# Kernel optimization log

Hardware: AMD Instinct MI355X
Metric: run time of the kernel (lower is better)

Reference implementation:

```python
import jax, jax.numpy as jnp
import numpy as np

B, S, D = 4, 2048, 1024
H = 16
DH = D // H  # 64


def setup_inputs() -> dict:
    key = jax.random.key(0)
    ks = jax.random.split(key, 9)
    s = 0.02
    return {
        "x": jax.random.normal(ks[0], (B, S, D), dtype=jnp.float32),
        "Wq": jax.random.normal(ks[1], (D, D), dtype=jnp.float32) * s,
        "bq": jnp.zeros((D,), dtype=jnp.float32),
        "Wk": jax.random.normal(ks[2], (D, D), dtype=jnp.float32) * s,
        "bk": jnp.zeros((D,), dtype=jnp.float32),
        "Wv": jax.random.normal(ks[3], (D, D), dtype=jnp.float32) * s,
        "bv": jnp.zeros((D,), dtype=jnp.float32),
        "Wp": jax.random.normal(ks[4], (D, D), dtype=jnp.float32) * s,
        "bp": jnp.zeros((D,), dtype=jnp.float32),
    }


def reference(x, Wq, bq, Wk, bk, Wv, bv, Wp, bp):
    b, s, d = x.shape
    # projections (torch Linear: x @ W.T + b)
    q = (x @ Wq.T + bq).reshape(b, s, H, DH).transpose(0, 2, 1, 3)   # [B,H,S,DH]
    # quirk faithful to source: key viewed as (B,S,DH,H) then transpose(1,3) -> [B,H,DH,S]
    k = (x @ Wk.T + bk).reshape(b, s, DH, H).transpose(0, 3, 2, 1)   # [B,H,DH,S]
    v = (x @ Wv.T + bv).reshape(b, s, H, DH).transpose(0, 2, 1, 3)   # [B,H,S,DH]

    scale = 1.0 / np.sqrt(DH).astype(np.float32)
    scores = jnp.einsum('bhqd,bhds->bhqs', q, k) * scale             # [B,H,S,S]
    causal = jnp.tril(jnp.ones((s, s), dtype=bool))
    scores = jnp.where(causal, scores, -jnp.inf)
    attn = jax.nn.softmax(scores, axis=-1)
    out = jnp.einsum('bhqs,bhsd->bhqd', attn, v)                      # [B,H,S,DH]
    out = out.transpose(0, 2, 1, 3).reshape(b, s, d)                  # [B,S,D]
    return out @ Wp.T + bp
```

## Files before the change

kernel.cpp:

```cpp
#include <hip/hip_runtime.h>
#include <cstdint>

#define B_  4
#define S_  2048
#define D_  1024
#define H_  16
#define DH_ 64

typedef unsigned short u16;
typedef __attribute__((ext_vector_type(8))) __bf16 bf16x8;
typedef __attribute__((ext_vector_type(4))) float f32x4;
typedef __attribute__((ext_vector_type(2))) uint32_t u32x2;

__device__ __forceinline__ u16 f2bf(float f) {
    union { float f; uint32_t u; } v; v.f = f;
    uint32_t r = (v.u + 0x7FFFu + ((v.u >> 16) & 1u)) >> 16;
    return (u16)r;
}
__device__ __forceinline__ u16 f2bf_fast(float f) {
    union { float f; uint32_t u; } v; v.f = f;
    return (u16)((v.u + 0x8000u) >> 16);
}
__device__ __forceinline__ uint32_t cvtpk(float lo, float hi) {
    uint32_t r;
    asm("v_cvt_pk_bf16_f32 %0, %1, %2" : "=v"(r) : "v"(lo), "v"(hi));
    return r;
}
__device__ __forceinline__ void gl2lds16(const void* g, void* l) {
    __builtin_amdgcn_global_load_lds(
        (const __attribute__((address_space(1))) void*)g,
        (__attribute__((address_space(3))) void*)l,
        16, 0, 0);
}

__global__ __launch_bounds__(256) void cvt_kernel(
    const float* __restrict__ x,  const float* __restrict__ wq,
    const float* __restrict__ wk, const float* __restrict__ wv,
    const float* __restrict__ wp,
    u16* __restrict__ xb, u16* __restrict__ wqb, u16* __restrict__ wkb,
    u16* __restrict__ wvb, u16* __restrict__ wpb)
{
    int bid = blockIdx.x;
    const float* src; u16* dst; int base;
    if (bid < 8192) {
        src = x; dst = xb; base = bid;
    } else {
        int w = (bid - 8192) >> 10;
        base  = (bid - 8192) & 1023;
        switch (w) {
            case 0: src = wq; dst = wqb; break;
            case 1: src = wk; dst = wkb; break;
            case 2: src = wv; dst = wvb; break;
            default: src = wp; dst = wpb; break;
        }
    }
    size_t i4 = (size_t)base * 256 + threadIdx.x;
    float4 v = *(const float4*)(src + i4 * 4);
    ushort4 o;
    o.x = f2bf(v.x); o.y = f2bf(v.y); o.z = f2bf(v.z); o.w = f2bf(v.w);
    *(ushort4*)(dst + i4 * 4) = o;
}

__device__ __forceinline__ void gemm_core(
    u16* sA, u16* sB,
    const u16* __restrict__ X, const u16* __restrict__ W,
    const float* __restrict__ bias,
    u16* __restrict__ out_bf, float* __restrict__ out_f,
    int m0, int n0, int kperm, int mode, float scale)
{
    const int tid  = threadIdx.x;
    const int lane = tid & 63;
    const int wave = tid >> 6;
    const int l16  = lane & 15, l4 = lane >> 4;

    f32x4 acc[4][4];
#pragma unroll
    for (int i = 0; i < 4; ++i)
#pragma unroll
        for (int j = 0; j < 4; ++j)
            acc[i][j] = (f32x4){0.f, 0.f, 0.f, 0.f};

    const int wm = (wave >> 1) * 64;
    const int wn = (wave & 1) * 64;

    for (int k0 = 0; k0 < 1024; k0 += 64) {
#pragma unroll
        for (int t = 0; t < 4; ++t) {
            int idx = wave * 256 + t * 64 + lane;
            int row = idx >> 3, scc = idx & 7;
            int cg  = scc ^ (row & 7);
            gl2lds16(X + (size_t)(m0 + row) * 1024 + k0 + cg * 8,
                     &sA[(wave * 256 + t * 64) * 8]);
        }
#pragma unroll
        for (int t = 0; t < 4; ++t) {
            int idx = wave * 256 + t * 64 + lane;
            int row = idx >> 3, scc = idx & 7;
            int cg  = scc ^ (row & 7);
            int n   = n0 + row;
            int wr  = kperm ? ((n & 63) * 16 + (n >> 6)) : n;
            gl2lds16(W + (size_t)wr * 1024 + k0 + cg * 8,
                     &sB[(wave * 256 + t * 64) * 8]);
        }
        __syncthreads();

#pragma unroll
        for (int kk = 0; kk < 2; ++kk) {
            bf16x8 a[4], b[4];
#pragma unroll
            for (int i = 0; i < 4; ++i) {
                int row = wm + i * 16 + l16;
                int ch  = (kk * 4 + l4) ^ (row & 7);
                a[i] = *(const bf16x8*)&sA[row * 64 + ch * 8];
            }
#pragma unroll
            for (int j = 0; j < 4; ++j) {
                int row = wn + j * 16 + l16;
                int ch  = (kk * 4 + l4) ^ (row & 7);
                b[j] = *(const bf16x8*)&sB[row * 64 + ch * 8];
            }
#pragma unroll
            for (int i = 0; i < 4; ++i)
#pragma unroll
                for (int j = 0; j < 4; ++j)
                    acc[i][j] = __builtin_amdgcn_mfma_f32_16x16x32_bf16(
                        a[i], b[j], acc[i][j], 0, 0, 0);
        }
        __syncthreads();
    }

    float bj[4];
#pragma unroll
    for (int j = 0; j < 4; ++j) {
        int n  = n0 + wn + j * 16 + l16;
        int wr = kperm ? ((n & 63) * 16 + (n >> 6)) : n;
        bj[j]  = bias[wr];
    }
#pragma unroll
    for (int i = 0; i < 4; ++i) {
#pragma unroll
        for (int j = 0; j < 4; ++j) {
#pragma unroll
            for (int r = 0; r < 4; ++r) {
                int m = m0 + wm + i * 16 + l4 * 4 + r;
                int n = n0 + wn + j * 16 + l16;
                float v = (acc[i][j][r] + bj[j]) * scale;
                int bb = m >> 11, s = m & 2047;
                int h = n >> 6, dh = n & 63;
                if (mode == 1) {
                    out_bf[(((size_t)bb * H_ + h) * S_ + s) * DH_ + dh] = f2bf(v);
                } else if (mode == 2) {
                    out_bf[(((size_t)bb * H_ + h) * DH_ + dh) * S_ + s] = f2bf(v);
                } else {
                    out_f[(size_t)m * 1024 + n] = v;
                }
            }
        }
    }
}

__global__ __launch_bounds__(256, 4) void qkv_kernel(
    const u16* __restrict__ xb,
    const u16* __restrict__ Wqb, const float* __restrict__ bq,
    const u16* __restrict__ Wkb, const float* __restrict__ bk,
    const u16* __restrict__ Wvb, const float* __restrict__ bv,
    u16* __restrict__ Q, u16* __restrict__ K, u16* __restrict__ V)
{
    __shared__ __align__(16) u16 sA[128 * 64];
    __shared__ __align__(16) u16 sB[128 * 64];
    int swz = (blockIdx.x & 7) * 192 + (blockIdx.x >> 3);
    int x = swz & 7, y = (swz >> 3) & 63, z = swz >> 9;
    int n0 = x * 128, m0 = y * 128;
    const u16* W = (z == 0) ? Wqb : (z == 1) ? Wkb : Wvb;
    const float* bi = (z == 0) ? bq : (z == 1) ? bk : bv;
    u16* out = (z == 0) ? Q : (z == 1) ? K : V;
    const float c = 0.18033688011112042f;
    gemm_core(sA, sB, xb, W, bi, out, nullptr, m0, n0,
              (z == 1) ? 1 : 0, (z == 2) ? 2 : 1, (z == 0) ? c : 1.0f);
}

__global__ __launch_bounds__(256, 4) void proj_kernel(
    const u16* __restrict__ Ob, const u16* __restrict__ Wpb,
    const float* __restrict__ bp, float* __restrict__ out)
{
    __shared__ __align__(16) u16 sA[128 * 64];
    __shared__ __align__(16) u16 sB[128 * 64];
    int swz = (blockIdx.x & 7) * 64 + (blockIdx.x >> 3);
    int x = swz & 7, y = swz >> 3;
    gemm_core(sA, sB, Ob, Wpb, bp, nullptr, out,
              y * 128, x * 128, 0, 0, 1.0f);
}

#define LDP 72
__global__ __launch_bounds__(256, 4) void attn_flash(
    const u16* __restrict__ Q, const u16* __restrict__ K,
    const u16* __restrict__ Vt, u16* __restrict__ O)
{
    const int tid  = threadIdx.x;
    const int lane = tid & 63;
    const int wave = tid >> 6;
    const int l16  = lane & 15, l4 = lane >> 4;
    int swz = (blockIdx.x & 7) * 128 + (blockIdx.x >> 3);
    const int qt   = swz & 15;
    const int bh   = swz >> 4;

    __shared__ __align__(16) u16 sK[64 * LDP];
    __shared__ __align__(16) u16 sVt[64 * LDP];
    __shared__ __align__(16) u16 sP[4][16 * LDP];

    const int b = bh >> 4, h = bh & 15;

    const int srow = tid >> 3, scc = tid & 7;
    const u16* Kbase = K  + (size_t)bh * S_ * DH_;
    const u16* Vbase = Vt + (size_t)bh * DH_ * S_;

#pragma unroll 1
    for (int half = 0; half < 2; ++half) {
        const int q0 = (half ? (31 - qt) : qt) * 64;

        bf16x8 aq[2];
        {
            const u16* qp = Q + ((size_t)bh * S_ + q0 + wave * 16 + l16) * DH_ + l4 * 8;
            aq[0] = *(const bf16x8*)qp;
            aq[1] = *(const bf16x8*)(qp + 32);
        }

        float lsum = 0.f;
        f32x4 o[4];
#pragma unroll
        for (int dt = 0; dt < 4; ++dt) o[dt] = (f32x4){0.f, 0.f, 0.f, 0.f};

        uint4 pk0, pk1, pv0, pv1;
        pk0 = *(const uint4*)(Kbase + (size_t)(srow)      * DH_ + scc * 8);
        pk1 = *(const uint4*)(Kbase + (size_t)(srow + 32) * DH_ + scc * 8);
        pv0 = *(const uint4*)(Vbase + (size_t)(srow)      * S_  + scc * 8);
        pv1 = *(const uint4*)(Vbase + (size_t)(srow + 32) * S_  + scc * 8);

        for (int k0 = 0; k0 <= q0; k0 += 64) {
            *(uint4*)&sK [(srow)      * LDP + scc * 8] = pk0;
            *(uint4*)&sK [(srow + 32) * LDP + scc * 8] = pk1;
            *(uint4*)&sVt[(srow)      * LDP + scc * 8] = pv0;
            *(uint4*)&sVt[(srow + 32) * LDP + scc * 8] = pv1;
            if (k0 + 64 <= q0) {
                int kn = k0 + 64;
                pk0 = *(const uint4*)(Kbase + (size_t)(kn + srow)      * DH_ + scc * 8);
                pk1 = *(const uint4*)(Kbase + (size_t)(kn + srow + 32) * DH_ + scc * 8);
                pv0 = *(const uint4*)(Vbase + (size_t)(srow)      * S_ + kn + scc * 8);
                pv1 = *(const uint4*)(Vbase + (size_t)(srow + 32) * S_ + kn + scc * 8);
            }
            __syncthreads();

            f32x4 ts[4];
#pragma unroll
            for (int ct = 0; ct < 4; ++ct) {
                f32x4 sacc = (f32x4){0.f, 0.f, 0.f, 0.f};
#pragma unroll
                for (int kk = 0; kk < 2; ++kk) {
                    bf16x8 ak = *(const bf16x8*)&sK[(ct * 16 + l16) * LDP + kk * 32 + l4 * 8];
                    sacc = __builtin_amdgcn_mfma_f32_16x16x32_bf16(ak, aq[kk], sacc, 0, 0, 0);
                }
                ts[ct] = sacc;
            }

            if (k0 == q0) {
#pragma unroll
                for (int ct = 0; ct < 4; ++ct)
#pragma unroll
                    for (int r = 0; r < 4; ++r) {
                        int key = ct * 16 + l4 * 4 + r;
                        int qr  = wave * 16 + l16;
                        if (key > qr) ts[ct][r] = -1e30f;
                    }
            }

            uint32_t pw[4][2];
#pragma unroll
            for (int ct = 0; ct < 4; ++ct) {
                float p0 = exp2f(ts[ct][0]);
                float p1 = exp2f(ts[ct][1]);
                float p2 = exp2f(ts[ct][2]);
                float p3 = exp2f(ts[ct][3]);
                lsum += (p0 + p1) + (p2 + p3);
                pw[ct][0] = cvtpk(p0, p1);
                pw[ct][1] = cvtpk(p2, p3);
            }
#pragma unroll
            for (int ct = 0; ct < 4; ++ct)
                *(u32x2*)&sP[wave][l16 * LDP + ct * 16 + l4 * 4] =
                    *(const u32x2*)pw[ct];
            asm volatile("s_waitcnt lgkmcnt(0)" ::: "memory");

#pragma unroll
            for (int kk = 0; kk < 2; ++kk) {
                bf16x8 ap = *(const bf16x8*)&sP[wave][l16 * LDP + kk * 32 + l4 * 8];
#pragma unroll
                for (int dt = 0; dt < 4; ++dt) {
                    bf16x8 bv = *(const bf16x8*)&sVt[(dt * 16 + l16) * LDP + kk * 32 + l4 * 8];
                    o[dt] = __builtin_amdgcn_mfma_f32_16x16x32_bf16(ap, bv, o[dt], 0, 0, 0);
                }
            }
            __syncthreads();
        }

        lsum += __shfl_xor(lsum, 16, 64);
        lsum += __shfl_xor(lsum, 32, 64);
        float linv = 1.0f / lsum;
        float inv[4];
#pragma unroll
        for (int r = 0; r < 4; ++r) inv[r] = __shfl(linv, (l4 << 2) + r, 16);

#pragma unroll
        for (int dt = 0; dt < 4; ++dt) {
#pragma unroll
            for (int r = 0; r < 4; ++r) {
                int s  = q0 + wave * 16 + l4 * 4 + r;
                int dh = dt * 16 + l16;
                O[((size_t)b * S_ + s) * D_ + h * 64 + dh] = f2bf_fast(o[dt][r] * inv[r]);
            }
        }
    }
}

extern "C" void kernel_launch(void* const* d_in, const int* in_sizes, int n_in,
                              void* d_out, int out_size, void* d_ws, size_t ws_size,
                              hipStream_t stream) {
    const float* x  = (const float*)d_in[0];
    const float* Wq = (const float*)d_in[1];
    const float* bq = (const float*)d_in[2];
    const float* Wk = (const float*)d_in[3];
    const float* bk = (const float*)d_in[4];
    const float* Wv = (const float*)d_in[5];
    const float* bv = (const float*)d_in[6];
    const float* Wp = (const float*)d_in[7];
    const float* bp = (const float*)d_in[8];

    u16* ws = (u16*)d_ws;
    const size_t xel = (size_t)B_ * S_ * D_;
    const size_t wel = (size_t)D_ * D_;
    u16* xb  = ws;
    u16* Wqb = xb + xel;
    u16* Wkb = Wqb + wel;
    u16* Wvb = Wkb + wel;
    u16* Wpb = Wvb + wel;
    u16* Q   = Wpb + wel;
    u16* Kb  = Q + xel;
    u16* Vtb = Kb + xel;
    u16* Ob  = Vtb + xel;

    cvt_kernel<<<dim3(12288), dim3(256), 0, stream>>>(
        x, Wq, Wk, Wv, Wp, xb, Wqb, Wkb, Wvb, Wpb);
    qkv_kernel<<<dim3(1536), dim3(256), 0, stream>>>(
        xb, Wqb, bq, Wkb, bk, Wvb, bv, Q, Kb, Vtb);
    attn_flash<<<dim3(1024), dim3(256), 0, stream>>>(Q, Kb, Vtb, Ob);
    proj_kernel<<<dim3(512), dim3(256), 0, stream>>>(Ob, Wpb, bp, (float*)d_out);
}
```

Baseline: 273.7 us.

## Widen QKV GEMM tile to 128x256 with per-wave 128x64 outputs

The QKV projection now uses 128x256 block tiles, with each wave computing a 128x64 slab (8x4 MFMA tiles), which halves the grid to 768 blocks. The goal is more reuse of each A fragment and fewer redundant global loads of X. The output projection keeps a specialised 128x128 path that writes fp32 directly. The cost is double the accumulator registers and LDS per block, with launch bounds lowered to 2 blocks per CU, which reduces occupancy and latency hiding.

After: 285.9 us. 1.04x slower.

```diff
diff --git a/kernel.cpp b/kernel.cpp
--- a/kernel.cpp
+++ b/kernel.cpp
@@ -61,11 +61,11 @@
     *(ushort4*)(dst + i4 * 4) = o;
 }
 
-__device__ __forceinline__ void gemm_core(
+__device__ __forceinline__ void gemm_wide(
     u16* sA, u16* sB,
     const u16* __restrict__ X, const u16* __restrict__ W,
     const float* __restrict__ bias,
-    u16* __restrict__ out_bf, float* __restrict__ out_f,
+    u16* __restrict__ out_bf,
     int m0, int n0, int kperm, int mode, float scale)
 {
     const int tid  = threadIdx.x;
@@ -73,15 +73,14 @@
     const int wave = tid >> 6;
     const int l16  = lane & 15, l4 = lane >> 4;
 
-    f32x4 acc[4][4];
-#pragma unroll
-    for (int i = 0; i < 4; ++i)
+    f32x4 acc[8][4];
+#pragma unroll
+    for (int i = 0; i < 8; ++i)
 #pragma unroll
         for (int j = 0; j < 4; ++j)
             acc[i][j] = (f32x4){0.f, 0.f, 0.f, 0.f};
 
-    const int wm = (wave >> 1) * 64;
-    const int wn = (wave & 1) * 64;
+    const int wn = wave * 64;
 
     for (int k0 = 0; k0 < 1024; k0 += 64) {
 #pragma unroll
@@ -93,23 +92,23 @@
                      &sA[(wave * 256 + t * 64) * 8]);
         }
 #pragma unroll
-        for (int t = 0; t < 4; ++t) {
-            int idx = wave * 256 + t * 64 + lane;
+        for (int t = 0; t < 8; ++t) {
+            int idx = wave * 512 + t * 64 + lane;
             int row = idx >> 3, scc = idx & 7;
             int cg  = scc ^ (row & 7);
             int n   = n0 + row;
             int wr  = kperm ? ((n & 63) * 16 + (n >> 6)) : n;
             gl2lds16(W + (size_t)wr * 1024 + k0 + cg * 8,
-                     &sB[(wave * 256 + t * 64) * 8]);
+                     &sB[(wave * 512 + t * 64) * 8]);
         }
         __syncthreads();
 
 #pragma unroll
         for (int kk = 0; kk < 2; ++kk) {
-            bf16x8 a[4], b[4];
-#pragma unroll
-            for (int i = 0; i < 4; ++i) {
-                int row = wm + i * 16 + l16;
+            bf16x8 a[8], b[4];
+#pragma unroll
+            for (int i = 0; i < 8; ++i) {
+                int row = i * 16 + l16;
                 int ch  = (kk * 4 + l4) ^ (row & 7);
                 a[i] = *(const bf16x8*)&sA[row * 64 + ch * 8];
             }
@@ -120,7 +119,7 @@
                 b[j] = *(const bf16x8*)&sB[row * 64 + ch * 8];
             }
 #pragma unroll
-            for (int i = 0; i < 4; ++i)
+            for (int i = 0; i < 8; ++i)
 #pragma unroll
                 for (int j = 0; j < 4; ++j)
                     acc[i][j] = __builtin_amdgcn_mfma_f32_16x16x32_bf16(
@@ -137,29 +136,111 @@
         bj[j]  = bias[wr];
     }
 #pragma unroll
-    for (int i = 0; i < 4; ++i) {
+    for (int i = 0; i < 8; ++i) {
 #pragma unroll
         for (int j = 0; j < 4; ++j) {
 #pragma unroll
             for (int r = 0; r < 4; ++r) {
-                int m = m0 + wm + i * 16 + l4 * 4 + r;
+                int m = m0 + i * 16 + l4 * 4 + r;
                 int n = n0 + wn + j * 16 + l16;
                 float v = (acc[i][j][r] + bj[j]) * scale;
                 int bb = m >> 11, s = m & 2047;
                 int h = n >> 6, dh = n & 63;
                 if (mode == 1) {
                     out_bf[(((size_t)bb * H_ + h) * S_ + s) * DH_ + dh] = f2bf(v);
-                } else if (mode == 2) {
+                } else {
                     out_bf[(((size_t)bb * H_ + h) * DH_ + dh) * S_ + s] = f2bf(v);
-                } else {
-                    out_f[(size_t)m * 1024 + n] = v;
                 }
             }
         }
     }
 }
 
-__global__ __launch_bounds__(256, 4) void qkv_kernel(
+__device__ __forceinline__ void gemm_core(
+    u16* sA, u16* sB,
+    const u16* __restrict__ X, const u16* __restrict__ W,
+    const float* __restrict__ bias,
+    float* __restrict__ out_f,
+    int m0, int n0)
+{
+    const int tid  = threadIdx.x;
+    const int lane = tid & 63;
+    const int wave = tid >> 6;
+    const int l16  = lane & 15, l4 = lane >> 4;
+
+    f32x4 acc[4][4];
+#pragma unroll
+    for (int i = 0; i < 4; ++i)
+#pragma unroll
+        for (int j = 0; j < 4; ++j)
+            acc[i][j] = (f32x4){0.f, 0.f, 0.f, 0.f};
+
+    const int wm = (wave >> 1) * 64;
+    const int wn = (wave & 1) * 64;
+
+    for (int k0 = 0; k0 < 1024; k0 += 64) {
+#pragma unroll
+        for (int t = 0; t < 4; ++t) {
+            int idx = wave * 256 + t * 64 + lane;
+            int row = idx >> 3, scc = idx & 7;
+            int cg  = scc ^ (row & 7);
+            gl2lds16(X + (size_t)(m0 + row) * 1024 + k0 + cg * 8,
+                     &sA[(wave * 256 + t * 64) * 8]);
+        }
+#pragma unroll
+        for (int t = 0; t < 4; ++t) {
+            int idx = wave * 256 + t * 64 + lane;
+            int row = idx >> 3, scc = idx & 7;
+            int cg  = scc ^ (row & 7);
+            gl2lds16(W + (size_t)(n0 + row) * 1024 + k0 + cg * 8,
+                     &sB[(wave * 256 + t * 64) * 8]);
+        }
+        __syncthreads();
+
+#pragma unroll
+        for (int kk = 0; kk < 2; ++kk) {
+            bf16x8 a[4], b[4];
+#pragma unroll
+            for (int i = 0; i < 4; ++i) {
+                int row = wm + i * 16 + l16;
+                int ch  = (kk * 4 + l4) ^ (row & 7);
+                a[i] = *(const bf16x8*)&sA[row * 64 + ch * 8];
+            }
+#pragma unroll
+            for (int j = 0; j < 4; ++j) {
+                int row = wn + j * 16 + l16;
+                int ch  = (kk * 4 + l4) ^ (row & 7);
+                b[j] = *(const bf16x8*)&sB[row * 64 + ch * 8];
+            }
+#pragma unroll
+            for (int i = 0; i < 4; ++i)
+#pragma unroll
+                for (int j = 0; j < 4; ++j)
+                    acc[i][j] = __builtin_amdgcn_mfma_f32_16x16x32_bf16(
+                        a[i], b[j], acc[i][j], 0, 0, 0);
+        }
+        __syncthreads();
+    }
+
+    float bj[4];
+#pragma unroll
+    for (int j = 0; j < 4; ++j)
+        bj[j] = bias[n0 + wn + j * 16 + l16];
+#pragma unroll
+    for (int i = 0; i < 4; ++i) {
+#pragma unroll
+        for (int j = 0; j < 4; ++j) {
+#pragma unroll
+            for (int r = 0; r < 4; ++r) {
+                int m = m0 + wm + i * 16 + l4 * 4 + r;
+                int n = n0 + wn + j * 16 + l16;
+                out_f[(size_t)m * 1024 + n] = acc[i][j][r] + bj[j];
+            }
+        }
+    }
+}
+
+__global__ __launch_bounds__(256, 2) void qkv_kernel(
     const u16* __restrict__ xb,
     const u16* __restrict__ Wqb, const float* __restrict__ bq,
     const u16* __restrict__ Wkb, const float* __restrict__ bk,
@@ -167,15 +248,15 @@
     u16* __restrict__ Q, u16* __restrict__ K, u16* __restrict__ V)
 {
     __shared__ __align__(16) u16 sA[128 * 64];
-    __shared__ __align__(16) u16 sB[128 * 64];
-    int swz = (blockIdx.x & 7) * 192 + (blockIdx.x >> 3);
-    int x = swz & 7, y = (swz >> 3) & 63, z = swz >> 9;
-    int n0 = x * 128, m0 = y * 128;
+    __shared__ __align__(16) u16 sB[256 * 64];
+    int swz = (blockIdx.x & 7) * 96 + (blockIdx.x >> 3);
+    int x = swz & 3, y = (swz >> 2) & 63, z = swz >> 8;
+    int n0 = x * 256, m0 = y * 128;
     const u16* W = (z == 0) ? Wqb : (z == 1) ? Wkb : Wvb;
     const float* bi = (z == 0) ? bq : (z == 1) ? bk : bv;
     u16* out = (z == 0) ? Q : (z == 1) ? K : V;
     const float c = 0.18033688011112042f;
-    gemm_core(sA, sB, xb, W, bi, out, nullptr, m0, n0,
+    gemm_wide(sA, sB, xb, W, bi, out, m0, n0,
               (z == 1) ? 1 : 0, (z == 2) ? 2 : 1, (z == 0) ? c : 1.0f);
 }
 
@@ -187,8 +268,7 @@
     __shared__ __align__(16) u16 sB[128 * 64];
     int swz = (blockIdx.x & 7) * 64 + (blockIdx.x >> 3);
     int x = swz & 7, y = swz >> 3;
-    gemm_core(sA, sB, Ob, Wpb, bp, nullptr, out,
-              y * 128, x * 128, 0, 0, 1.0f);
+    gemm_core(sA, sB, Ob, Wpb, bp, out, y * 128, x * 128);
 }
 
 #define LDP 72
@@ -349,7 +429,7 @@
 
     cvt_kernel<<<dim3(12288), dim3(256), 0, stream>>>(
         x, Wq, Wk, Wv, Wp, xb, Wqb, Wkb, Wvb, Wpb);
-    qkv_kernel<<<dim3(1536), dim3(256), 0, stream>>>(
+    qkv_kernel<<<dim3(768), dim3(256), 0, stream>>>(
         xb, Wqb, bq, Wkb, bk, Wvb, bv, Q, Kb, Vtb);
     attn_flash<<<dim3(1024), dim3(256), 0, stream>>>(Q, Kb, Vtb, Ob);
     proj_kernel<<<dim3(512), dim3(256), 0, stream>>>(Ob, Wpb, bp, (float*)d_out);
```

## Double-buffer LDS tiles in GEMM core to overlap loads with MFMA

Applied to the files above, without the earlier changes.

Splits the tile staging into a helper and doubles the shared-memory A/B buffers, so the next K-slice is prefetched into the alternate buffer while MFMAs run on the current one. This removes one barrier-exposed load latency per K-step in both the QKV and output projection GEMMs. The launch bounds occupancy hint drops from 4 to 2 blocks per CU because each block now uses twice the LDS. The loop is kept at unroll 1, so fewer resident waves are left to hide latency.

New measurement: 283.2 us. 1.03x slower.

```diff
diff --git a/kernel.cpp b/kernel.cpp
--- a/kernel.cpp
+++ b/kernel.cpp
@@ -61,6 +61,31 @@
     *(ushort4*)(dst + i4 * 4) = o;
 }
 
+__device__ __forceinline__ void stage_tiles(
+    u16* dA, u16* dB,
+    const u16* __restrict__ X, const u16* __restrict__ W,
+    int m0, int n0, int k0, int kperm, int wave, int lane)
+{
+#pragma unroll
+    for (int t = 0; t < 4; ++t) {
+        int idx = wave * 256 + t * 64 + lane;
+        int row = idx >> 3, scc = idx & 7;
+        int cg  = scc ^ (row & 7);
+        gl2lds16(X + (size_t)(m0 + row) * 1024 + k0 + cg * 8,
+                 &dA[(wave * 256 + t * 64) * 8]);
+    }
+#pragma unroll
+    for (int t = 0; t < 4; ++t) {
+        int idx = wave * 256 + t * 64 + lane;
+        int row = idx >> 3, scc = idx & 7;
+        int cg  = scc ^ (row & 7);
+        int n   = n0 + row;
+        int wr  = kperm ? ((n & 63) * 16 + (n >> 6)) : n;
+        gl2lds16(W + (size_t)wr * 1024 + k0 + cg * 8,
+                 &dB[(wave * 256 + t * 64) * 8]);
+    }
+}
+
 __device__ __forceinline__ void gemm_core(
     u16* sA, u16* sB,
     const u16* __restrict__ X, const u16* __restrict__ W,
@@ -83,27 +108,18 @@
     const int wm = (wave >> 1) * 64;
     const int wn = (wave & 1) * 64;
 
-    for (int k0 = 0; k0 < 1024; k0 += 64) {
-#pragma unroll
-        for (int t = 0; t < 4; ++t) {
-            int idx = wave * 256 + t * 64 + lane;
-            int row = idx >> 3, scc = idx & 7;
-            int cg  = scc ^ (row & 7);
-            gl2lds16(X + (size_t)(m0 + row) * 1024 + k0 + cg * 8,
-                     &sA[(wave * 256 + t * 64) * 8]);
-        }
-#pragma unroll
-        for (int t = 0; t < 4; ++t) {
-            int idx = wave * 256 + t * 64 + lane;
-            int row = idx >> 3, scc = idx & 7;
-            int cg  = scc ^ (row & 7);
-            int n   = n0 + row;
-            int wr  = kperm ? ((n & 63) * 16 + (n >> 6)) : n;
-            gl2lds16(W + (size_t)wr * 1024 + k0 + cg * 8,
-                     &sB[(wave * 256 + t * 64) * 8]);
-        }
-        __syncthreads();
-
+    stage_tiles(sA, sB, X, W, m0, n0, 0, kperm, wave, lane);
+    __syncthreads();
+
+    int cur = 0;
+#pragma unroll 1
+    for (int t = 0; t < 16; ++t) {
+        if (t < 15)
+            stage_tiles(sA + (cur ^ 1) * 8192, sB + (cur ^ 1) * 8192,
+                        X, W, m0, n0, (t + 1) * 64, kperm, wave, lane);
+
+        const u16* cA = sA + cur * 8192;
+        const u16* cB = sB + cur * 8192;
 #pragma unroll
         for (int kk = 0; kk < 2; ++kk) {
             bf16x8 a[4], b[4];
@@ -111,13 +127,13 @@
             for (int i = 0; i < 4; ++i) {
                 int row = wm + i * 16 + l16;
                 int ch  = (kk * 4 + l4) ^ (row & 7);
-                a[i] = *(const bf16x8*)&sA[row * 64 + ch * 8];
+                a[i] = *(const bf16x8*)&cA[row * 64 + ch * 8];
             }
 #pragma unroll
             for (int j = 0; j < 4; ++j) {
                 int row = wn + j * 16 + l16;
                 int ch  = (kk * 4 + l4) ^ (row & 7);
-                b[j] = *(const bf16x8*)&sB[row * 64 + ch * 8];
+                b[j] = *(const bf16x8*)&cB[row * 64 + ch * 8];
             }
 #pragma unroll
             for (int i = 0; i < 4; ++i)
@@ -127,6 +143,7 @@
                         a[i], b[j], acc[i][j], 0, 0, 0);
         }
         __syncthreads();
+        cur ^= 1;
     }
 
     float bj[4];
@@ -159,15 +176,15 @@
     }
 }
 
-__global__ __launch_bounds__(256, 4) void qkv_kernel(
+__global__ __launch_bounds__(256, 2) void qkv_kernel(
     const u16* __restrict__ xb,
     const u16* __restrict__ Wqb, const float* __restrict__ bq,
     const u16* __restrict__ Wkb, const float* __restrict__ bk,
     const u16* __restrict__ Wvb, const float* __restrict__ bv,
     u16* __restrict__ Q, u16* __restrict__ K, u16* __restrict__ V)
 {
-    __shared__ __align__(16) u16 sA[128 * 64];
-    __shared__ __align__(16) u16 sB[128 * 64];
+    __shared__ __align__(16) u16 sA[2 * 128 * 64];
+    __shared__ __align__(16) u16 sB[2 * 128 * 64];
     int swz = (blockIdx.x & 7) * 192 + (blockIdx.x >> 3);
     int x = swz & 7, y = (swz >> 3) & 63, z = swz >> 9;
     int n0 = x * 128, m0 = y * 128;
@@ -179,12 +196,12 @@
               (z == 1) ? 1 : 0, (z == 2) ? 2 : 1, (z == 0) ? c : 1.0f);
 }
 
-__global__ __launch_bounds__(256, 4) void proj_kernel(
+__global__ __launch_bounds__(256, 2) void proj_kernel(
     const u16* __restrict__ Ob, const u16* __restrict__ Wpb,
     const float* __restrict__ bp, float* __restrict__ out)
 {
-    __shared__ __align__(16) u16 sA[128 * 64];
-    __shared__ __align__(16) u16 sB[128 * 64];
+    __shared__ __align__(16) u16 sA[2 * 128 * 64];
+    __shared__ __align__(16) u16 sB[2 * 128 * 64];
     int swz = (blockIdx.x & 7) * 64 + (blockIdx.x >> 3);
     int x = swz & 7, y = swz >> 3;
     gemm_core(sA, sB, Ob, Wpb, bp, nullptr, out,
```

## Share K/V tile loads across paired query tiles in causal attention

Applied to the files above, without the earlier changes.

Each block previously processed its two query tiles (qt and 31-qt) one after the other, streaming K/V from the start for each. Now both query tiles run in a single key loop: every staged K/V tile feeds the far tile, and the near tile too while it is still inside its causal range. This cuts global K/V loads and barriers for the shorter tile roughly in half. The cost is more live registers (two accumulator sets and two Q fragments), which may lower occupancy.

Result: slower. 286.2 us (+4.6%).

```diff
diff --git a/kernel.cpp b/kernel.cpp
--- a/kernel.cpp
+++ b/kernel.cpp
@@ -214,101 +214,112 @@
     const u16* Kbase = K  + (size_t)bh * S_ * DH_;
     const u16* Vbase = Vt + (size_t)bh * DH_ * S_;
 
-#pragma unroll 1
-    for (int half = 0; half < 2; ++half) {
-        const int q0 = (half ? (31 - qt) : qt) * 64;
-
-        bf16x8 aq[2];
-        {
-            const u16* qp = Q + ((size_t)bh * S_ + q0 + wave * 16 + l16) * DH_ + l4 * 8;
-            aq[0] = *(const bf16x8*)qp;
-            aq[1] = *(const bf16x8*)(qp + 32);
-        }
-
-        float lsum = 0.f;
-        f32x4 o[4];
-#pragma unroll
-        for (int dt = 0; dt < 4; ++dt) o[dt] = (f32x4){0.f, 0.f, 0.f, 0.f};
-
-        uint4 pk0, pk1, pv0, pv1;
-        pk0 = *(const uint4*)(Kbase + (size_t)(srow)      * DH_ + scc * 8);
-        pk1 = *(const uint4*)(Kbase + (size_t)(srow + 32) * DH_ + scc * 8);
-        pv0 = *(const uint4*)(Vbase + (size_t)(srow)      * S_  + scc * 8);
-        pv1 = *(const uint4*)(Vbase + (size_t)(srow + 32) * S_  + scc * 8);
-
-        for (int k0 = 0; k0 <= q0; k0 += 64) {
-            *(uint4*)&sK [(srow)      * LDP + scc * 8] = pk0;
-            *(uint4*)&sK [(srow + 32) * LDP + scc * 8] = pk1;
-            *(uint4*)&sVt[(srow)      * LDP + scc * 8] = pv0;
-            *(uint4*)&sVt[(srow + 32) * LDP + scc * 8] = pv1;
-            if (k0 + 64 <= q0) {
-                int kn = k0 + 64;
-                pk0 = *(const uint4*)(Kbase + (size_t)(kn + srow)      * DH_ + scc * 8);
-                pk1 = *(const uint4*)(Kbase + (size_t)(kn + srow + 32) * DH_ + scc * 8);
-                pv0 = *(const uint4*)(Vbase + (size_t)(srow)      * S_ + kn + scc * 8);
-                pv1 = *(const uint4*)(Vbase + (size_t)(srow + 32) * S_ + kn + scc * 8);
-            }
-            __syncthreads();
-
-            f32x4 ts[4];
-#pragma unroll
-            for (int ct = 0; ct < 4; ++ct) {
-                f32x4 sacc = (f32x4){0.f, 0.f, 0.f, 0.f};
-#pragma unroll
-                for (int kk = 0; kk < 2; ++kk) {
-                    bf16x8 ak = *(const bf16x8*)&sK[(ct * 16 + l16) * LDP + kk * 32 + l4 * 8];
-                    sacc = __builtin_amdgcn_mfma_f32_16x16x32_bf16(ak, aq[kk], sacc, 0, 0, 0);
+    const int q0a = qt * 64;
+    const int q0b = (31 - qt) * 64;
+
+    bf16x8 aqA[2], aqB[2];
+    {
+        const u16* qp = Q + ((size_t)bh * S_ + q0a + wave * 16 + l16) * DH_ + l4 * 8;
+        aqA[0] = *(const bf16x8*)qp;
+        aqA[1] = *(const bf16x8*)(qp + 32);
+    }
+    {
+        const u16* qp = Q + ((size_t)bh * S_ + q0b + wave * 16 + l16) * DH_ + l4 * 8;
+        aqB[0] = *(const bf16x8*)qp;
+        aqB[1] = *(const bf16x8*)(qp + 32);
+    }
+
+    float lsumA = 0.f, lsumB = 0.f;
+    f32x4 oA[4], oB[4];
+#pragma unroll
+    for (int dt = 0; dt < 4; ++dt) {
+        oA[dt] = (f32x4){0.f, 0.f, 0.f, 0.f};
+        oB[dt] = (f32x4){0.f, 0.f, 0.f, 0.f};
+    }
+
+    auto tile_half = [&](const bf16x8* aq, f32x4* o, float& lsum, bool diag) {
+        f32x4 ts[4];
+#pragma unroll
+        for (int ct = 0; ct < 4; ++ct) {
+            f32x4 sacc = (f32x4){0.f, 0.f, 0.f, 0.f};
+#pragma unroll
+            for (int kk = 0; kk < 2; ++kk) {
+                bf16x8 ak = *(const bf16x8*)&sK[(ct * 16 + l16) * LDP + kk * 32 + l4 * 8];
+                sacc = __builtin_amdgcn_mfma_f32_16x16x32_bf16(ak, aq[kk], sacc, 0, 0, 0);
+            }
+            ts[ct] = sacc;
+        }
+        if (diag) {
+#pragma unroll
+            for (int ct = 0; ct < 4; ++ct)
+#pragma unroll
+                for (int r = 0; r < 4; ++r) {
+                    int key = ct * 16 + l4 * 4 + r;
+                    int qr  = wave * 16 + l16;
+                    if (key > qr) ts[ct][r] = -1e30f;
                 }
-                ts[ct] = sacc;
-            }
-
-            if (k0 == q0) {
-#pragma unroll
-                for (int ct = 0; ct < 4; ++ct)
-#pragma unroll
-                    for (int r = 0; r < 4; ++r) {
-                        int key = ct * 16 + l4 * 4 + r;
-                        int qr  = wave * 16 + l16;
-                        if (key > qr) ts[ct][r] = -1e30f;
-                    }
-            }
-
-            uint32_t pw[4][2];
-#pragma unroll
-            for (int ct = 0; ct < 4; ++ct) {
-                float p0 = exp2f(ts[ct][0]);
-                float p1 = exp2f(ts[ct][1]);
-                float p2 = exp2f(ts[ct][2]);
-                float p3 = exp2f(ts[ct][3]);
-                lsum += (p0 + p1) + (p2 + p3);
-                pw[ct][0] = cvtpk(p0, p1);
-                pw[ct][1] = cvtpk(p2, p3);
-            }
-#pragma unroll
-            for (int ct = 0; ct < 4; ++ct)
-                *(u32x2*)&sP[wave][l16 * LDP + ct * 16 + l4 * 4] =
-                    *(const u32x2*)pw[ct];
-            asm volatile("s_waitcnt lgkmcnt(0)" ::: "memory");
-
-#pragma unroll
-            for (int kk = 0; kk < 2; ++kk) {
-                bf16x8 ap = *(const bf16x8*)&sP[wave][l16 * LDP + kk * 32 + l4 * 8];
-#pragma unroll
-                for (int dt = 0; dt < 4; ++dt) {
-                    bf16x8 bv = *(const bf16x8*)&sVt[(dt * 16 + l16) * LDP + kk * 32 + l4 * 8];
-                    o[dt] = __builtin_amdgcn_mfma_f32_16x16x32_bf16(ap, bv, o[dt], 0, 0, 0);
-                }
-            }
-            __syncthreads();
-        }
-
+        }
+        uint32_t pw[4][2];
+#pragma unroll
+        for (int ct = 0; ct < 4; ++ct) {
+            float p0 = exp2f(ts[ct][0]);
+            float p1 = exp2f(ts[ct][1]);
+            float p2 = exp2f(ts[ct][2]);
+            float p3 = exp2f(ts[ct][3]);
+            lsum += (p0 + p1) + (p2 + p3);
+            pw[ct][0] = cvtpk(p0, p1);
+            pw[ct][1] = cvtpk(p2, p3);
+        }
+#pragma unroll
+        for (int ct = 0; ct < 4; ++ct)
+            *(u32x2*)&sP[wave][l16 * LDP + ct * 16 + l4 * 4] =
+                *(const u32x2*)pw[ct];
+        asm volatile("s_waitcnt lgkmcnt(0)" ::: "memory");
+#pragma unroll
+        for (int kk = 0; kk < 2; ++kk) {
+            bf16x8 ap = *(const bf16x8*)&sP[wave][l16 * LDP + kk * 32 + l4 * 8];
+#pragma unroll
+            for (int dt = 0; dt < 4; ++dt) {
+                bf16x8 bv = *(const bf16x8*)&sVt[(dt * 16 + l16) * LDP + kk * 32 + l4 * 8];
+                o[dt] = __builtin_amdgcn_mfma_f32_16x16x32_bf16(ap, bv, o[dt], 0, 0, 0);
+            }
+        }
+    };
+
+    uint4 pk0, pk1, pv0, pv1;
+    pk0 = *(const uint4*)(Kbase + (size_t)(srow)      * DH_ + scc * 8);
+    pk1 = *(const uint4*)(Kbase + (size_t)(srow + 32) * DH_ + scc * 8);
+    pv0 = *(const uint4*)(Vbase + (size_t)(srow)      * S_  + scc * 8);
+    pv1 = *(const uint4*)(Vbase + (size_t)(srow + 32) * S_  + scc * 8);
+
+    for (int k0 = 0; k0 <= q0b; k0 += 64) {
+        *(uint4*)&sK [(srow)      * LDP + scc * 8] = pk0;
+        *(uint4*)&sK [(srow + 32) * LDP + scc * 8] = pk1;
+        *(uint4*)&sVt[(srow)      * LDP + scc * 8] = pv0;
+        *(uint4*)&sVt[(srow + 32) * LDP + scc * 8] = pv1;
+        if (k0 + 64 <= q0b) {
+            int kn = k0 + 64;
+            pk0 = *(const uint4*)(Kbase + (size_t)(kn + srow)      * DH_ + scc * 8);
+            pk1 = *(const uint4*)(Kbase + (size_t)(kn + srow + 32) * DH_ + scc * 8);
+            pv0 = *(const uint4*)(Vbase + (size_t)(srow)      * S_ + kn + scc * 8);
+            pv1 = *(const uint4*)(Vbase + (size_t)(srow + 32) * S_ + kn + scc * 8);
+        }
+        __syncthreads();
+
+        tile_half(aqB, oB, lsumB, k0 == q0b);
+        if (k0 <= q0a)
+            tile_half(aqA, oA, lsumA, k0 == q0a);
+
+        __syncthreads();
+    }
+
+    auto epilogue = [&](int q0, const f32x4* o, float lsum) {
         lsum += __shfl_xor(lsum, 16, 64);
         lsum += __shfl_xor(lsum, 32, 64);
         float linv = 1.0f / lsum;
         float inv[4];
 #pragma unroll
         for (int r = 0; r < 4; ++r) inv[r] = __shfl(linv, (l4 << 2) + r, 16);
-
 #pragma unroll
         for (int dt = 0; dt < 4; ++dt) {
 #pragma unroll
@@ -318,7 +329,9 @@
                 O[((size_t)b * S_ + s) * D_ + h * 64 + dh] = f2bf_fast(o[dt][r] * inv[r]);
             }
         }
-    }
+    };
+    epilogue(q0b, oB, lsumB);
+    epilogue(q0a, oA, lsumA);
 }
 
 extern "C" void kernel_launch(void* const* d_in, const int* in_sizes, int n_in,
```
